# Kernel optimization log

Hardware: AMD Instinct MI355X
Metric: run time of the kernel (lower is better)

## Reference

```python
import jax, jax.numpy as jnp
import numpy as np

N = 100000   # nodes
E = 1600000  # edges
IN = 128
HEADS = 4
D = 128 // HEADS  # per-head hidden (DGL: hid_feats/num_heads = 32)
OUT = 64
NEG_SLOPE = 0.2


def gat_conv(h, src, dst, W, al, ar, b, apply_relu):
    """DGL-style GATConv. h:[N,F_in], W:[F_in,H*D], al/ar:[H,D], b:[H*D]."""
    Hn, Dd = al.shape
    ft = (h @ W).reshape(-1, Hn, Dd)                      # [N,H,D]
    el = jnp.sum(ft * al, axis=-1)                        # [N,H]
    er = jnp.sum(ft * ar, axis=-1)                        # [N,H]
    e = jax.nn.leaky_relu(el[src] + er[dst], NEG_SLOPE)   # [E,H]
    # edge softmax over incoming edges of each dst node (numerically stable)
    emax = jax.ops.segment_max(e, dst, num_segments=N)    # [N,H]
    ex = jnp.exp(e - emax[dst])                           # [E,H]
    denom = jax.ops.segment_sum(ex, dst, num_segments=N)  # [N,H]
    alpha = ex / denom[dst]                               # [E,H]
    msg = ft[src] * alpha[:, :, None]                     # [E,H,D]
    out = jax.ops.segment_sum(msg, dst, num_segments=N)   # [N,H,D]
    out = out + b.reshape(Hn, Dd)
    if apply_relu:
        out = jax.nn.relu(out)
    return out.reshape(-1, Hn * Dd)                       # flatten(1)


def setup_inputs() -> dict:
    key = jax.random.key(0)
    ks = jax.random.split(key, 16)
    features = jax.random.normal(ks[0], (N, IN), dtype=jnp.float32)
    src = jax.random.randint(ks[1], (E,), 0, N, dtype=jnp.int32)
    # guarantee every node has at least one in-edge (allow_zero_in_degree=False)
    dst = jnp.concatenate([jnp.arange(N, dtype=jnp.int32),
                           jax.random.randint(ks[2], (E - N,), 0, N, dtype=jnp.int32)])
    s = 0.05
    return {
        "features": features, "src": src, "dst": dst,
        "W0": jax.random.normal(ks[3], (IN, HEADS * D)) * s,
        "al0": jax.random.normal(ks[4], (HEADS, D)) * s,
        "ar0": jax.random.normal(ks[5], (HEADS, D)) * s,
        "b0": jnp.zeros((HEADS * D,), jnp.float32),
        "W1": jax.random.normal(ks[6], (HEADS * D, HEADS * D)) * s,
        "al1": jax.random.normal(ks[7], (HEADS, D)) * s,
        "ar1": jax.random.normal(ks[8], (HEADS, D)) * s,
        "b1": jnp.zeros((HEADS * D,), jnp.float32),
        "W2": jax.random.normal(ks[9], (HEADS * D, OUT)) * s,
        "al2": jax.random.normal(ks[10], (1, OUT)) * s,
        "ar2": jax.random.normal(ks[11], (1, OUT)) * s,
        "b2": jnp.zeros((OUT,), jnp.float32),
    }


def reference(features, src, dst, W0, al0, ar0, b0, W1, al1, ar1, b1, W2, al2, ar2, b2):
    # dropout is identity at inference time
    h = gat_conv(features, src, dst, W0, al0, ar0, b0, apply_relu=True)
    h = gat_conv(h, src, dst, W1, al1, ar1, b1, apply_relu=True)
    h = gat_conv(h, src, dst, W2, al2, ar2, b2, apply_relu=False)  # last layer: 1 head, no activation
    return h  # [N, OUT]
```

## Files before the change

### kernel.cpp

```cpp
#include <hip/hip_runtime.h>
#include <hip/hip_bf16.h>
#include <hip/hip_fp16.h>
#include <math.h>


constexpr int KDIM = 128;
constexpr int BSH = 9;
constexpr int EPB = 4096;


__global__ __launch_bounds__(256) void ehist(const int* __restrict__ dst,
                                             int* __restrict__ cmat,
                                             int E, int nebs) {
    __shared__ int lh[256];
    const int t = threadIdx.x;
    lh[t] = 0;
    __syncthreads();
    const int base = blockIdx.x * EPB;
    const int cntE = min(EPB, E - base);
    for (int i = t; i < cntE; i += 256) atomicAdd(&lh[dst[base + i] >> BSH], 1);
    __syncthreads();
    cmat[t * nebs + blockIdx.x] = lh[t];
}

__global__ __launch_bounds__(512) void bscan(int* __restrict__ cmat,
                                             int* __restrict__ rowtot, int nebs) {
    __shared__ int sh[512];
    const int b = blockIdx.x, t = threadIdx.x;
    int v = (t < nebs) ? cmat[b * nebs + t] : 0;
    sh[t] = v;
    __syncthreads();
    for (int off = 1; off < 512; off <<= 1) {
        int u = (t >= off) ? sh[t - off] : 0;
        __syncthreads();
        sh[t] += u;
        __syncthreads();
    }
    if (t < nebs) cmat[b * nebs + t] = sh[t] - v;
    if (t == 511) rowtot[b] = sh[511];
}

__global__ __launch_bounds__(256) void bbase_scan(const int* __restrict__ rowtot,
                                                  int* __restrict__ bbase) {
    __shared__ int sh[256];
    const int t = threadIdx.x;
    int v = rowtot[t];
    sh[t] = v;
    __syncthreads();
    for (int off = 1; off < 256; off <<= 1) {
        int u = (t >= off) ? sh[t - off] : 0;
        __syncthreads();
        sh[t] += u;
        __syncthreads();
    }
    bbase[t] = sh[t] - v;
}

__global__ __launch_bounds__(256) void escatter(
    const int* __restrict__ src, const int* __restrict__ dst,
    const int* __restrict__ cmat, const int* __restrict__ bbase,
    unsigned long long* __restrict__ ebuf, int E, int nebs) {
    __shared__ unsigned long long sbuf[EPB];
    __shared__ int lh[256], lstart[256], lcur[256];
    const int t = threadIdx.x;
    const int base = blockIdx.x * EPB;
    const int cntE = min(EPB, E - base);

    lh[t] = 0;
    __syncthreads();
    for (int i = t; i < cntE; i += 256) atomicAdd(&lh[dst[base + i] >> BSH], 1);
    __syncthreads();
    {
        __shared__ int sh[256];
        int v = lh[t];
        sh[t] = v;
        __syncthreads();
        for (int off = 1; off < 256; off <<= 1) {
            int u = (t >= off) ? sh[t - off] : 0;
            __syncthreads();
            sh[t] += u;
            __syncthreads();
        }
        lstart[t] = sh[t] - v;
        lcur[t] = sh[t] - v;
    }
    __syncthreads();
    for (int i = t; i < cntE; i += 256) {
        int d = dst[base + i], s = src[base + i];
        int r = atomicAdd(&lcur[d >> BSH], 1);
        sbuf[r] = ((unsigned long long)d << 32) | (unsigned int)s;
    }
    __syncthreads();
    for (int j = t; j < cntE; j += 256) {
        unsigned long long v = sbuf[j];
        int bk = (int)(v >> 32) >> BSH;
        int gpos = bbase[bk] + cmat[bk * nebs + blockIdx.x] + (j - lstart[bk]);
        ebuf[gpos] = v;
    }
}

__global__ __launch_bounds__(512) void bucket_fill(
    const unsigned long long* __restrict__ ebuf, const int* __restrict__ bbase,
    int* __restrict__ rowptr, int* __restrict__ colx, int N, int E, int nbuck) {
    __shared__ int cnt[512], nxtl[512], sh[512];
    const int b = blockIdx.x, t = threadIdx.x;
    const int nodebase = b << BSH;
    const int nn = min(512, N - nodebase);
    const int estart = bbase[b];
    const int eend = (b + 1 < 256) ? bbase[b + 1] : E;

    cnt[t] = 0;
    __syncthreads();
    for (int i = estart + t; i < eend; i += 512)
        atomicAdd(&cnt[(int)(ebuf[i] >> 32) - nodebase], 1);
    __syncthreads();
    int v = cnt[t];
    sh[t] = v;
    __syncthreads();
    for (int off = 1; off < 512; off <<= 1) {
        int u = (t >= off) ? sh[t - off] : 0;
        __syncthreads();
        sh[t] += u;
        __syncthreads();
    }
    if (t < nn) rowptr[nodebase + t + 1] = estart + sh[t];
    if (b == 0 && t == 0) rowptr[0] = 0;
    nxtl[t] = estart + sh[t] - v;
    __syncthreads();
    for (int i = estart + t; i < eend; i += 512) {
        unsigned long long v2 = ebuf[i];
        int d = (int)(v2 >> 32) - nodebase;
        int pos = atomicAdd(&nxtl[d], 1);
        colx[pos] = (int)(unsigned int)v2;
    }
}


template <int FOUT, int H, bool HOUT>
__global__ __launch_bounds__(256, 4) void gemm_ft(
    const float* __restrict__ hin, const float* __restrict__ W,
    const float* __restrict__ al, const float* __restrict__ ar,
    void* __restrict__ ftout, float* __restrict__ el, float* __restrict__ er,
    int nnodes) {
    constexpr int BK = 16;
    constexpr int LDH = 132;
    constexpr int TN = (FOUT == 128) ? 8 : 4;
    constexpr int WCH = BK * FOUT / 1024;

    __shared__ float ht[2][BK * LDH];
    __shared__ float Ws[2][BK * FOUT];

    const int tid = threadIdx.x;
    const int nb = blockIdx.x * 128;
    const int tc = tid & 15, row = tid >> 4;
    const int nl = tid >> 2;
    const int kq = (tid & 3) * 4;

    float4 hreg[2];
    float4 wreg[WCH];

    auto load_chunk = [&](int k0) {
#pragma unroll
        for (int it = 0; it < 2; ++it) {
            int n = nb + nl + it * 64;
            hreg[it] = (n < nnodes)
                           ? *(const float4*)&hin[(size_t)n * KDIM + k0 + kq]
                           : make_float4(0.f, 0.f, 0.f, 0.f);
        }
        const float4* Wg = (const float4*)&W[(size_t)k0 * FOUT];
#pragma unroll
        for (int it = 0; it < WCH; ++it) wreg[it] = Wg[tid + it * 256];
    };
    auto store_chunk = [&](int b) {
#pragma unroll
        for (int it = 0; it < 2; ++it) {
            int nn = nl + it * 64;
            ht[b][(kq + 0) * LDH + nn] = hreg[it].x;
            ht[b][(kq + 1) * LDH + nn] = hreg[it].y;
            ht[b][(kq + 2) * LDH + nn] = hreg[it].z;
            ht[b][(kq + 3) * LDH + nn] = hreg[it].w;
        }
#pragma unroll
        for (int it = 0; it < WCH; ++it)
            ((float4*)Ws[b])[tid + it * 256] = wreg[it];
    };

    float acc[8][TN];
#pragma unroll
    for (int m = 0; m < 8; ++m)
#pragma unroll
        for (int j = 0; j < TN; ++j) acc[m][j] = 0.f;

    load_chunk(0);
    store_chunk(0);
    __syncthreads();

    for (int k0 = 0; k0 < KDIM / BK; ++k0) {
        const int cur = k0 & 1;
        if (k0 < KDIM / BK - 1) load_chunk((k0 + 1) * BK);

#pragma unroll 4
        for (int kk = 0; kk < BK; ++kk) {
            const float* hb = &ht[cur][kk * LDH];
            float4 h0 = *(const float4*)&hb[row * 4];
            float4 h1 = *(const float4*)&hb[64 + row * 4];
            float hv[8] = {h0.x, h0.y, h0.z, h0.w, h1.x, h1.y, h1.z, h1.w};
            const float* wb = &Ws[cur][kk * FOUT];
            float4 w0 = *(const float4*)&wb[tc * 4];
            float wv[TN];
            wv[0] = w0.x; wv[1] = w0.y; wv[2] = w0.z; wv[3] = w0.w;
            if constexpr (FOUT == 128) {
                float4 w1 = *(const float4*)&wb[64 + tc * 4];
                wv[4] = w1.x; wv[5] = w1.y; wv[6] = w1.z; wv[7] = w1.w;
            }
#pragma unroll
            for (int m = 0; m < 8; ++m)
#pragma unroll
                for (int j = 0; j < TN; ++j)
                    acc[m][j] = fmaf(hv[m], wv[j], acc[m][j]);
        }
        if (k0 < KDIM / BK - 1) store_chunk(cur ^ 1);
        __syncthreads();
    }

    float alv[TN], arv[TN];
#pragma unroll
    for (int j = 0; j < 4; ++j) {
        alv[j] = al[tc * 4 + j];
        arv[j] = ar[tc * 4 + j];
    }
    if constexpr (FOUT == 128) {
#pragma unroll
        for (int j = 0; j < 4; ++j) {
            alv[4 + j] = al[64 + tc * 4 + j];
            arv[4 + j] = ar[64 + tc * 4 + j];
        }
    }

#pragma unroll
    for (int m = 0; m < 8; ++m) {
        const int r = (m < 4) ? (row * 4 + m) : (64 + row * 4 + m - 4);
        const int n = nb + r;
        const bool valid = n < nnodes;

        float pl0 = 0.f, pr0 = 0.f, pl1 = 0.f, pr1 = 0.f;
#pragma unroll
        for (int j = 0; j < 4; ++j) {
            pl0 = fmaf(acc[m][j], alv[j], pl0);
            pr0 = fmaf(acc[m][j], arv[j], pr0);
        }
        if constexpr (FOUT == 128) {
#pragma unroll
            for (int j = 0; j < 4; ++j) {
                pl1 = fmaf(acc[m][4 + j], alv[4 + j], pl1);
                pr1 = fmaf(acc[m][4 + j], arv[4 + j], pr1);
            }
        }

        if constexpr (H == 4) {
#pragma unroll
            for (int msk = 1; msk < 8; msk <<= 1) {
                pl0 += __shfl_xor(pl0, msk);
                pr0 += __shfl_xor(pr0, msk);
                pl1 += __shfl_xor(pl1, msk);
                pr1 += __shfl_xor(pr1, msk);
            }
            if (valid && (tc == 0 || tc == 8)) {
                int hbase = (tc == 0) ? 0 : 1;
                el[(size_t)n * 4 + hbase] = pl0;
                er[(size_t)n * 4 + hbase] = pr0;
                el[(size_t)n * 4 + hbase + 2] = pl1;
                er[(size_t)n * 4 + hbase + 2] = pr1;
            }
        } else {
#pragma unroll
            for (int msk = 1; msk < 16; msk <<= 1) {
                pl0 += __shfl_xor(pl0, msk);
                pr0 += __shfl_xor(pr0, msk);
            }
            if (valid && tc == 0) {
                el[n] = pl0;
                er[n] = pr0;
            }
        }

        if (valid) {
            if constexpr (HOUT) {
                __half* fth = (__half*)ftout;
                ushort4 u0;
                u0.x = __half_as_ushort(__float2half_rn(acc[m][0]));
                u0.y = __half_as_ushort(__float2half_rn(acc[m][1]));
                u0.z = __half_as_ushort(__float2half_rn(acc[m][2]));
                u0.w = __half_as_ushort(__float2half_rn(acc[m][3]));
                *(ushort4*)&fth[(size_t)n * FOUT + tc * 4] = u0;
                if constexpr (FOUT == 128) {
                    ushort4 u1;
                    u1.x = __half_as_ushort(__float2half_rn(acc[m][4]));
                    u1.y = __half_as_ushort(__float2half_rn(acc[m][5]));
                    u1.z = __half_as_ushort(__float2half_rn(acc[m][6]));
                    u1.w = __half_as_ushort(__float2half_rn(acc[m][7]));
                    *(ushort4*)&fth[(size_t)n * FOUT + 64 + tc * 4] = u1;
                }
            } else {
                float* ftf = (float*)ftout;
                *(float4*)&ftf[(size_t)n * FOUT + tc * 4] =
                    make_float4(acc[m][0], acc[m][1], acc[m][2], acc[m][3]);
                if constexpr (FOUT == 128)
                    *(float4*)&ftf[(size_t)n * FOUT + 64 + tc * 4] =
                        make_float4(acc[m][4], acc[m][5], acc[m][6], acc[m][7]);
            }
        }
    }
}


template <int F, int H, bool RELU, bool HIN>
__global__ __launch_bounds__(256) void gat_aggregate(
    const int* __restrict__ rowptr, const int* __restrict__ colx,
    const float* __restrict__ el, const float* __restrict__ er,
    const void* __restrict__ ftv, const float* __restrict__ bias,
    float* __restrict__ out, int nnodes) {
    constexpr int CPL = F / 16;
    const int tid = threadIdx.x, wv = tid >> 6, lane = tid & 63;
    const int grp = lane >> 4, sub = lane & 15;
    const int n = blockIdx.x * 16 + wv * 4 + grp;
    const bool valid = n < nnodes;
    const int nn = valid ? n : 0;

    const int start = rowptr[nn];
    const int end = valid ? rowptr[nn + 1] : start;
    int md = end - start;
    md = max(md, __shfl_xor(md, 16));
    md = max(md, __shfl_xor(md, 32));
    const int nit = (md + 7) / 8;

    const int head = (H == 4) ? (sub >> 2) : 0;
    const float er_s = (H == 4) ? er[(size_t)nn * 4 + head] : er[nn];

    float sA = 0.f, sB = 0.f;
    float acc[CPL];
#pragma unroll
    for (int c = 0; c < CPL; ++c) acc[c] = 0.f;

    int idxA[4], idxB[4];
    float xA[4], xB[4];
    uint4 hA[4], hB[4];
    float4 fA[4], fB[4];

    auto issue = [&](int (&idxX)[4], float (&xX)[4], uint4 (&hX)[4],
                     float4 (&fX)[4], int e0) {
#pragma unroll
        for (int i = 0; i < 4; ++i) {
            int ee = e0 + i;
            idxX[i] = (ee < end) ? colx[ee] : -1;
        }
#pragma unroll
        for (int i = 0; i < 4; ++i) {
            int sn = (idxX[i] < 0) ? 0 : idxX[i];
            if constexpr (HIN) {
                const __half* fth = (const __half*)ftv;
                hX[i] = *(const uint4*)&fth[(size_t)sn * F + sub * 8];
            } else {
                const float* ftf = (const float*)ftv;
                fX[i] = *(const float4*)&ftf[(size_t)sn * F + sub * 4];
            }
            xX[i] = (H == 4) ? el[(size_t)sn * 4 + head] : el[sn];
        }
    };
    auto compute = [&](int (&idxX)[4], float (&xX)[4], uint4 (&hX)[4],
                       float4 (&fX)[4], float& sX) {
#pragma unroll
        for (int i = 0; i < 4; ++i) {
            float x = xX[i] + er_s;
            x = fmaxf(x, 0.2f * x);
            float p = __expf(x);
            p = (idxX[i] >= 0) ? p : 0.f;
            sX += p;
            if constexpr (HIN) {
                const __half* hv = (const __half*)&hX[i];
#pragma unroll
                for (int c = 0; c < CPL; ++c)
                    acc[c] = fmaf(p, __half2float(hv[c]), acc[c]);
            } else {
                acc[0] = fmaf(p, fX[i].x, acc[0]);
                acc[1] = fmaf(p, fX[i].y, acc[1]);
                acc[2] = fmaf(p, fX[i].z, acc[2]);
                acc[3] = fmaf(p, fX[i].w, acc[3]);
            }
        }
    };

    int e0 = start;
    issue(idxA, xA, hA, fA, e0);
    for (int it = 0; it < nit; ++it) {
        issue(idxB, xB, hB, fB, e0 + 4);
        compute(idxA, xA, hA, fA, sA);
        issue(idxA, xA, hA, fA, e0 + 8);
        compute(idxB, xB, hB, fB, sB);
        e0 += 8;
    }

    if (!valid) return;
    float s = sA + sB;
    float inv = 1.0f / s;
    float o[CPL];
#pragma unroll
    for (int c = 0; c < CPL; ++c) {
        o[c] = acc[c] * inv + bias[sub * CPL + c];
        if (RELU) o[c] = fmaxf(o[c], 0.f);
    }
    if constexpr (CPL == 8) {
        *(float4*)&out[(size_t)n * F + sub * 8] =
            make_float4(o[0], o[1], o[2], o[3]);
        *(float4*)&out[(size_t)n * F + sub * 8 + 4] =
            make_float4(o[4], o[5], o[6], o[7]);
    } else {
        *(float4*)&out[(size_t)n * F + sub * 4] =
            make_float4(o[0], o[1], o[2], o[3]);
    }
}


static inline size_t alignup(size_t x) { return (x + 255) & ~(size_t)255; }

extern "C" void kernel_launch(void* const* d_in, const int* in_sizes, int n_in,
                              void* d_out, int out_size, void* d_ws, size_t ws_size,
                              hipStream_t stream) {
    const float* features = (const float*)d_in[0];
    const int* src = (const int*)d_in[1];
    const int* dst = (const int*)d_in[2];
    const float* W0 = (const float*)d_in[3];
    const float* al0 = (const float*)d_in[4];
    const float* ar0 = (const float*)d_in[5];
    const float* b0 = (const float*)d_in[6];
    const float* W1 = (const float*)d_in[7];
    const float* al1 = (const float*)d_in[8];
    const float* ar1 = (const float*)d_in[9];
    const float* b1 = (const float*)d_in[10];
    const float* W2 = (const float*)d_in[11];
    const float* al2 = (const float*)d_in[12];
    const float* ar2 = (const float*)d_in[13];
    const float* b2 = (const float*)d_in[14];
    float* out = (float*)d_out;

    const int N = in_sizes[0] / 128;
    const int E = in_sizes[1];
    const int nebs = (E + EPB - 1) / EPB;
    const int nbuck = (N + 511) >> BSH;

    char* w = (char*)d_ws;
    int* rowptr = (int*)w;     w += alignup((size_t)(N + 1) * 4);
    int* colx = (int*)w;       w += alignup((size_t)E * 4);
    float* ft32 = (float*)w;   w += alignup((size_t)N * 64 * 4);
    __half* ft16 = (__half*)w; w += alignup((size_t)N * 128 * 2);
    float* hbuf = (float*)w;   w += alignup((size_t)N * 128 * 4);
    float* el = (float*)w;     w += alignup((size_t)N * 4 * 4);
    float* er = (float*)w;     w += alignup((size_t)N * 4 * 4);
    unsigned long long* ebuf = (unsigned long long*)w;
    w += alignup((size_t)E * 8);
    int* cmat = (int*)w;       w += alignup((size_t)256 * nebs * 4);
    int* rowtot = (int*)w;     w += alignup(256 * 4);
    int* bbase = (int*)w;      w += alignup(256 * 4);

    hipMemsetAsync(rowtot, 0, 256 * 4, stream);
    ehist<<<nebs, 256, 0, stream>>>(dst, cmat, E, nebs);
    bscan<<<nbuck, 512, 0, stream>>>(cmat, rowtot, nebs);
    bbase_scan<<<1, 256, 0, stream>>>(rowtot, bbase);
    escatter<<<nebs, 256, 0, stream>>>(src, dst, cmat, bbase, ebuf, E, nebs);
    bucket_fill<<<nbuck, 512, 0, stream>>>(ebuf, bbase, rowptr, colx, N, E, nbuck);

    const int gGemm = (N + 127) / 128;
    const int gAgg = (N + 15) / 16;

    gemm_ft<128, 4, true><<<gGemm, 256, 0, stream>>>(features, W0, al0, ar0, ft16, el, er, N);
    gat_aggregate<128, 4, true, true><<<gAgg, 256, 0, stream>>>(rowptr, colx, el, er, ft16, b0, hbuf, N);

    gemm_ft<128, 4, true><<<gGemm, 256, 0, stream>>>(hbuf, W1, al1, ar1, ft16, el, er, N);
    gat_aggregate<128, 4, true, true><<<gAgg, 256, 0, stream>>>(rowptr, colx, el, er, ft16, b1, hbuf, N);

    gemm_ft<64, 1, false><<<gGemm, 256, 0, stream>>>(hbuf, W2, al2, ar2, ft32, el, er, N);
    gat_aggregate<64, 1, false, false><<<gAgg, 256, 0, stream>>>(rowptr, colx, el, er, ft32, b2, out, N);
}
```

Measured before the change: 395.1 us.

## Replace FP32 SIMT GEMM with split-bf16 MFMA GEMM using pre-swizzled weights

Replaces the scalar FMA node-feature GEMM with a matrix-core kernel built on 16x16x32 bf16 MFMA. Each operand is split into a bf16 hi part and a bf16 lo part, and three MFMAs per tile keep accuracy close to fp32. Weights are split and swizzled into the MFMA lane layout by a small prep kernel, and activations are converted into LDS in the same layout. This targets the compute-bound FP32 GEMM, at the cost of extra conversion work, scalar (non-vectorized) output stores, and a smaller 64-node tile.

```diff
diff --git a/kernel.cpp b/kernel.cpp
--- a/kernel.cpp
+++ b/kernel.cpp
@@ -4,9 +4,20 @@
 #include <math.h>
 
 
-constexpr int KDIM = 128;
 constexpr int BSH = 9;
 constexpr int EPB = 4096;
+
+typedef __attribute__((ext_vector_type(8))) short bf16x8;
+typedef __attribute__((ext_vector_type(4))) float f32x4;
+
+__device__ __forceinline__ ushort bf16_rne(float f) {
+    unsigned u = __float_as_uint(f);
+    u += 0x7FFF + ((u >> 16) & 1);
+    return (ushort)(u >> 16);
+}
+__device__ __forceinline__ float bf16_tof(ushort h) {
+    return __uint_as_float(((unsigned)h) << 16);
+}
 
 
 __global__ __launch_bounds__(256) void ehist(const int* __restrict__ dst,
@@ -136,178 +147,172 @@
 }
 
 
+template <int FOUT>
+__global__ __launch_bounds__(256) void wprep(const float* __restrict__ W,
+                                             ushort* __restrict__ wsw) {
+    constexpr int NT = FOUT / 16;
+    int idx = blockIdx.x * 256 + threadIdx.x;
+    if (idx >= 128 * FOUT / 4) return;
+    float4 v = ((const float4*)W)[idx];
+    int e0 = idx * 4;
+    int k = e0 / FOUT, c0 = e0 - k * FOUT;
+    int kstep = k >> 5, g = (k >> 3) & 3, i = k & 7;
+    float vv[4] = {v.x, v.y, v.z, v.w};
+#pragma unroll
+    for (int d = 0; d < 4; ++d) {
+        int c = c0 + d;
+        int tile = c >> 4, l16 = c & 15;
+        int lane = g * 16 + l16;
+        ushort hi = bf16_rne(vv[d]);
+        ushort lo = bf16_rne(vv[d] - bf16_tof(hi));
+        size_t base = ((((size_t)kstep * NT + tile) * 2 + 0) * 64 + lane) * 8 + i;
+        wsw[base] = hi;
+        wsw[base + 512] = lo;
+    }
+}
+
+
 template <int FOUT, int H, bool HOUT>
-__global__ __launch_bounds__(256, 4) void gemm_ft(
-    const float* __restrict__ hin, const float* __restrict__ W,
+__global__ __launch_bounds__(256) void gemm_mfma(
+    const float* __restrict__ hin, const ushort* __restrict__ wsw,
     const float* __restrict__ al, const float* __restrict__ ar,
     void* __restrict__ ftout, float* __restrict__ el, float* __restrict__ er,
     int nnodes) {
-    constexpr int BK = 16;
-    constexpr int LDH = 132;
-    constexpr int TN = (FOUT == 128) ? 8 : 4;
-    constexpr int WCH = BK * FOUT / 1024;
-
-    __shared__ float ht[2][BK * LDH];
-    __shared__ float Ws[2][BK * FOUT];
+    constexpr int NT = FOUT / 16;
+    constexpr int WHALF = 2 * NT * 2 * 64 * 8;
+    __shared__ ushort Asw[4 * 4 * 2 * 64 * 8];
+    __shared__ ushort Wsw[WHALF];
 
     const int tid = threadIdx.x;
-    const int nb = blockIdx.x * 128;
-    const int tc = tid & 15, row = tid >> 4;
-    const int nl = tid >> 2;
-    const int kq = (tid & 3) * 4;
-
-    float4 hreg[2];
-    float4 wreg[WCH];
-
-    auto load_chunk = [&](int k0) {
-#pragma unroll
-        for (int it = 0; it < 2; ++it) {
-            int n = nb + nl + it * 64;
-            hreg[it] = (n < nnodes)
-                           ? *(const float4*)&hin[(size_t)n * KDIM + k0 + kq]
-                           : make_float4(0.f, 0.f, 0.f, 0.f);
-        }
-        const float4* Wg = (const float4*)&W[(size_t)k0 * FOUT];
-#pragma unroll
-        for (int it = 0; it < WCH; ++it) wreg[it] = Wg[tid + it * 256];
-    };
-    auto store_chunk = [&](int b) {
-#pragma unroll
-        for (int it = 0; it < 2; ++it) {
-            int nn = nl + it * 64;
-            ht[b][(kq + 0) * LDH + nn] = hreg[it].x;
-            ht[b][(kq + 1) * LDH + nn] = hreg[it].y;
-            ht[b][(kq + 2) * LDH + nn] = hreg[it].z;
-            ht[b][(kq + 3) * LDH + nn] = hreg[it].w;
-        }
-#pragma unroll
-        for (int it = 0; it < WCH; ++it)
-            ((float4*)Ws[b])[tid + it * 256] = wreg[it];
-    };
-
-    float acc[8][TN];
-#pragma unroll
-    for (int m = 0; m < 8; ++m)
-#pragma unroll
-        for (int j = 0; j < TN; ++j) acc[m][j] = 0.f;
-
-    load_chunk(0);
-    store_chunk(0);
-    __syncthreads();
-
-    for (int k0 = 0; k0 < KDIM / BK; ++k0) {
-        const int cur = k0 & 1;
-        if (k0 < KDIM / BK - 1) load_chunk((k0 + 1) * BK);
-
-#pragma unroll 4
-        for (int kk = 0; kk < BK; ++kk) {
-            const float* hb = &ht[cur][kk * LDH];
-            float4 h0 = *(const float4*)&hb[row * 4];
-            float4 h1 = *(const float4*)&hb[64 + row * 4];
-            float hv[8] = {h0.x, h0.y, h0.z, h0.w, h1.x, h1.y, h1.z, h1.w};
-            const float* wb = &Ws[cur][kk * FOUT];
-            float4 w0 = *(const float4*)&wb[tc * 4];
-            float wv[TN];
-            wv[0] = w0.x; wv[1] = w0.y; wv[2] = w0.z; wv[3] = w0.w;
-            if constexpr (FOUT == 128) {
-                float4 w1 = *(const float4*)&wb[64 + tc * 4];
-                wv[4] = w1.x; wv[5] = w1.y; wv[6] = w1.z; wv[7] = w1.w;
-            }
-#pragma unroll
-            for (int m = 0; m < 8; ++m)
-#pragma unroll
-                for (int j = 0; j < TN; ++j)
-                    acc[m][j] = fmaf(hv[m], wv[j], acc[m][j]);
-        }
-        if (k0 < KDIM / BK - 1) store_chunk(cur ^ 1);
-        __syncthreads();
-    }
-
-    float alv[TN], arv[TN];
+    const int wv = tid >> 6, lane = tid & 63;
+    const int nb = blockIdx.x * 64;
+
+    {
+        const int nloc = tid >> 2;
+        const int qb = tid & 3;
+        const int gw = nloc >> 4, m = nloc & 15;
+        const int n = nb + nloc;
+        const bool v = n < nnodes;
+        const float4* hrow = (const float4*)&hin[(size_t)(v ? n : 0) * 128];
+#pragma unroll
+        for (int it = 0; it < 8; ++it) {
+            int q = qb + it * 4;
+            int k0 = q * 4;
+            float4 x = v ? hrow[q] : make_float4(0.f, 0.f, 0.f, 0.f);
+            int kstep = k0 >> 5, g = (k0 >> 3) & 3, i0 = k0 & 7;
+            int laneA = g * 16 + m;
+            size_t base =
+                ((((size_t)gw * 4 + kstep) * 2 + 0) * 64 + laneA) * 8 + i0;
+            float xs[4] = {x.x, x.y, x.z, x.w};
+            ushort4 uh, ul;
+            ushort h;
+            h = bf16_rne(xs[0]); uh.x = h; ul.x = bf16_rne(xs[0] - bf16_tof(h));
+            h = bf16_rne(xs[1]); uh.y = h; ul.y = bf16_rne(xs[1] - bf16_tof(h));
+            h = bf16_rne(xs[2]); uh.z = h; ul.z = bf16_rne(xs[2] - bf16_tof(h));
+            h = bf16_rne(xs[3]); uh.w = h; ul.w = bf16_rne(xs[3] - bf16_tof(h));
+            *(ushort4*)&Asw[base] = uh;
+            *(ushort4*)&Asw[base + 512] = ul;
+        }
+    }
+
+    f32x4 acc[NT];
+#pragma unroll
+    for (int t = 0; t < NT; ++t) acc[t] = (f32x4){0.f, 0.f, 0.f, 0.f};
+
+#pragma unroll
+    for (int kh = 0; kh < 2; ++kh) {
+        __syncthreads();
+        {
+            const uint4* srcp = (const uint4*)(wsw + (size_t)kh * WHALF);
+            uint4* dstp = (uint4*)Wsw;
+            constexpr int CNT = WHALF / 8;
+#pragma unroll
+            for (int ii = 0; ii < CNT / 256; ++ii)
+                dstp[tid + ii * 256] = srcp[tid + ii * 256];
+        }
+        __syncthreads();
+
+#pragma unroll
+        for (int ks2 = 0; ks2 < 2; ++ks2) {
+            const int kstep = kh * 2 + ks2;
+            bf16x8 ahi = *(const bf16x8*)
+                &Asw[(((wv * 4 + kstep) * 2 + 0) * 64 + lane) * 8];
+            bf16x8 alo = *(const bf16x8*)
+                &Asw[(((wv * 4 + kstep) * 2 + 1) * 64 + lane) * 8];
+#pragma unroll
+            for (int t = 0; t < NT; ++t) {
+                bf16x8 bhi = *(const bf16x8*)
+                    &Wsw[(((ks2 * NT + t) * 2 + 0) * 64 + lane) * 8];
+                bf16x8 blo = *(const bf16x8*)
+                    &Wsw[(((ks2 * NT + t) * 2 + 1) * 64 + lane) * 8];
+                acc[t] = __builtin_amdgcn_mfma_f32_16x16x32_bf16(ahi, bhi, acc[t], 0, 0, 0);
+                acc[t] = __builtin_amdgcn_mfma_f32_16x16x32_bf16(ahi, blo, acc[t], 0, 0, 0);
+                acc[t] = __builtin_amdgcn_mfma_f32_16x16x32_bf16(alo, bhi, acc[t], 0, 0, 0);
+            }
+        }
+    }
+
+    const int g = lane >> 4, l16 = lane & 15;
+    const int nrow0 = nb + wv * 16 + g * 4;
+
+    if constexpr (H == 4) {
+#pragma unroll
+        for (int h = 0; h < 4; ++h) {
+            float a0 = al[h * 32 + l16], a1 = al[h * 32 + 16 + l16];
+            float r0 = ar[h * 32 + l16], r1 = ar[h * 32 + 16 + l16];
+#pragma unroll
+            for (int j = 0; j < 4; ++j) {
+                float pl = acc[2 * h][j] * a0 + acc[2 * h + 1][j] * a1;
+                float pr = acc[2 * h][j] * r0 + acc[2 * h + 1][j] * r1;
+#pragma unroll
+                for (int msk = 1; msk < 16; msk <<= 1) {
+                    pl += __shfl_xor(pl, msk);
+                    pr += __shfl_xor(pr, msk);
+                }
+                int n = nrow0 + j;
+                if (l16 == 0 && n < nnodes) {
+                    el[(size_t)n * 4 + h] = pl;
+                    er[(size_t)n * 4 + h] = pr;
+                }
+            }
+        }
+    } else {
+#pragma unroll
+        for (int j = 0; j < 4; ++j) {
+            float pl = 0.f, pr = 0.f;
+#pragma unroll
+            for (int t = 0; t < NT; ++t) {
+                pl = fmaf(acc[t][j], al[t * 16 + l16], pl);
+                pr = fmaf(acc[t][j], ar[t * 16 + l16], pr);
+            }
+#pragma unroll
+            for (int msk = 1; msk < 16; msk <<= 1) {
+                pl += __shfl_xor(pl, msk);
+                pr += __shfl_xor(pr, msk);
+            }
+            int n = nrow0 + j;
+            if (l16 == 0 && n < nnodes) {
+                el[n] = pl;
+                er[n] = pr;
+            }
+        }
+    }
+
 #pragma unroll
     for (int j = 0; j < 4; ++j) {
-        alv[j] = al[tc * 4 + j];
-        arv[j] = ar[tc * 4 + j];
-    }
-    if constexpr (FOUT == 128) {
-#pragma unroll
-        for (int j = 0; j < 4; ++j) {
-            alv[4 + j] = al[64 + tc * 4 + j];
-            arv[4 + j] = ar[64 + tc * 4 + j];
-        }
-    }
-
-#pragma unroll
-    for (int m = 0; m < 8; ++m) {
-        const int r = (m < 4) ? (row * 4 + m) : (64 + row * 4 + m - 4);
-        const int n = nb + r;
-        const bool valid = n < nnodes;
-
-        float pl0 = 0.f, pr0 = 0.f, pl1 = 0.f, pr1 = 0.f;
-#pragma unroll
-        for (int j = 0; j < 4; ++j) {
-            pl0 = fmaf(acc[m][j], alv[j], pl0);
-            pr0 = fmaf(acc[m][j], arv[j], pr0);
-        }
-        if constexpr (FOUT == 128) {
-#pragma unroll
-            for (int j = 0; j < 4; ++j) {
-                pl1 = fmaf(acc[m][4 + j], alv[4 + j], pl1);
-                pr1 = fmaf(acc[m][4 + j], arv[4 + j], pr1);
-            }
-        }
-
-        if constexpr (H == 4) {
-#pragma unroll
-            for (int msk = 1; msk < 8; msk <<= 1) {
-                pl0 += __shfl_xor(pl0, msk);
-                pr0 += __shfl_xor(pr0, msk);
-                pl1 += __shfl_xor(pl1, msk);
-                pr1 += __shfl_xor(pr1, msk);
-            }
-            if (valid && (tc == 0 || tc == 8)) {
-                int hbase = (tc == 0) ? 0 : 1;
-                el[(size_t)n * 4 + hbase] = pl0;
-                er[(size_t)n * 4 + hbase] = pr0;
-                el[(size_t)n * 4 + hbase + 2] = pl1;
-                er[(size_t)n * 4 + hbase + 2] = pr1;
-            }
-        } else {
-#pragma unroll
-            for (int msk = 1; msk < 16; msk <<= 1) {
-                pl0 += __shfl_xor(pl0, msk);
-                pr0 += __shfl_xor(pr0, msk);
-            }
-            if (valid && tc == 0) {
-                el[n] = pl0;
-                er[n] = pr0;
-            }
-        }
-
-        if (valid) {
+        int n = nrow0 + j;
+        if (n < nnodes) {
             if constexpr (HOUT) {
                 __half* fth = (__half*)ftout;
-                ushort4 u0;
-                u0.x = __half_as_ushort(__float2half_rn(acc[m][0]));
-                u0.y = __half_as_ushort(__float2half_rn(acc[m][1]));
-                u0.z = __half_as_ushort(__float2half_rn(acc[m][2]));
-                u0.w = __half_as_ushort(__float2half_rn(acc[m][3]));
-                *(ushort4*)&fth[(size_t)n * FOUT + tc * 4] = u0;
-                if constexpr (FOUT == 128) {
-                    ushort4 u1;
-                    u1.x = __half_as_ushort(__float2half_rn(acc[m][4]));
-                    u1.y = __half_as_ushort(__float2half_rn(acc[m][5]));
-                    u1.z = __half_as_ushort(__float2half_rn(acc[m][6]));
-                    u1.w = __half_as_ushort(__float2half_rn(acc[m][7]));
-                    *(ushort4*)&fth[(size_t)n * FOUT + 64 + tc * 4] = u1;
-                }
+#pragma unroll
+                for (int t = 0; t < NT; ++t)
+                    fth[(size_t)n * FOUT + t * 16 + l16] =
+                        __float2half_rn(acc[t][j]);
             } else {
                 float* ftf = (float*)ftout;
-                *(float4*)&ftf[(size_t)n * FOUT + tc * 4] =
-                    make_float4(acc[m][0], acc[m][1], acc[m][2], acc[m][3]);
-                if constexpr (FOUT == 128)
-                    *(float4*)&ftf[(size_t)n * FOUT + 64 + tc * 4] =
-                        make_float4(acc[m][4], acc[m][5], acc[m][6], acc[m][7]);
+#pragma unroll
+                for (int t = 0; t < NT; ++t)
+                    ftf[(size_t)n * FOUT + t * 16 + l16] = acc[t][j];
             }
         }
     }
@@ -461,6 +466,9 @@
     int* cmat = (int*)w;       w += alignup((size_t)256 * nebs * 4);
     int* rowtot = (int*)w;     w += alignup(256 * 4);
     int* bbase = (int*)w;      w += alignup(256 * 4);
+    ushort* wsw0 = (ushort*)w; w += alignup(128 * 128 * 2 * 2);
+    ushort* wsw1 = (ushort*)w; w += alignup(128 * 128 * 2 * 2);
+    ushort* wsw2 = (ushort*)w; w += alignup(128 * 64 * 2 * 2);
 
     hipMemsetAsync(rowtot, 0, 256 * 4, stream);
     ehist<<<nebs, 256, 0, stream>>>(dst, cmat, E, nebs);
@@ -469,15 +477,19 @@
     escatter<<<nebs, 256, 0, stream>>>(src, dst, cmat, bbase, ebuf, E, nebs);
     bucket_fill<<<nbuck, 512, 0, stream>>>(ebuf, bbase, rowptr, colx, N, E, nbuck);
 
-    const int gGemm = (N + 127) / 128;
+    wprep<128><<<16, 256, 0, stream>>>(W0, wsw0);
+    wprep<128><<<16, 256, 0, stream>>>(W1, wsw1);
+    wprep<64><<<8, 256, 0, stream>>>(W2, wsw2);
+
+    const int gG = (N + 63) / 64;
     const int gAgg = (N + 15) / 16;
 
-    gemm_ft<128, 4, true><<<gGemm, 256, 0, stream>>>(features, W0, al0, ar0, ft16, el, er, N);
+    gemm_mfma<128, 4, true><<<gG, 256, 0, stream>>>(features, wsw0, al0, ar0, ft16, el, er, N);
     gat_aggregate<128, 4, true, true><<<gAgg, 256, 0, stream>>>(rowptr, colx, el, er, ft16, b0, hbuf, N);
 
-    gemm_ft<128, 4, true><<<gGemm, 256, 0, stream>>>(hbuf, W1, al1, ar1, ft16, el, er, N);
+    gemm_mfma<128, 4, true><<<gG, 256, 0, stream>>>(hbuf, wsw1, al1, ar1, ft16, el, er, N);
     gat_aggregate<128, 4, true, true><<<gAgg, 256, 0, stream>>>(rowptr, colx, el, er, ft16, b1, hbuf, N);
 
-    gemm_ft<64, 1, false><<<gGemm, 256, 0, stream>>>(hbuf, W2, al2, ar2, ft32, el, er, N);
+    gemm_mfma<64, 1, false><<<gG, 256, 0, stream>>>(hbuf, wsw2, al2, ar2, ft32, el, er, N);
     gat_aggregate<64, 1, false, false><<<gAgg, 256, 0, stream>>>(rowptr, colx, el, er, ft32, b2, out, N);
 }
```

Measured after the change: 363.6 us. 1.09x faster.
